# Optimization experiments

Hardware: AMD Instinct MI355X
Metric: run time of the kernel (lower is better)

Reference implementation:

```python
import jax, jax.numpy as jnp
import numpy as np

EPS = 1e-15
BN_EPS = 1e-5
N_NODES = 50000
N_EDGES = 800000
IN_CH = 32
OUT_CH = 32
DIM = 3


def _gmm_params(key, in_ch, out_ch, K):
    k1, k2, k3, k4 = jax.random.split(key, 4)
    g = jax.random.normal(k1, (in_ch, K * out_ch), jnp.float32) * (1.0 / np.sqrt(in_ch))
    mu = jax.random.normal(k2, (K, DIM), jnp.float32)
    sigma = jax.random.uniform(k3, (K, DIM), jnp.float32, 0.5, 1.5)
    root = jax.random.normal(k4, (in_ch, out_ch), jnp.float32) * (1.0 / np.sqrt(in_ch))
    bias = jnp.zeros((out_ch,), jnp.float32)
    return g, mu, sigma, root, bias


def setup_inputs() -> dict:
    key = jax.random.key(0)
    ks = jax.random.split(key, 12)
    x = jax.random.normal(ks[0], (N_NODES, IN_CH), jnp.float32)
    edge_index = jax.random.randint(ks[1], (2, N_EDGES), 0, N_NODES, jnp.int64)
    edge_attr = jax.random.uniform(ks[2], (N_EDGES, DIM), jnp.float32)
    g1, mu1, sig1, root1, b1 = _gmm_params(ks[3], IN_CH, OUT_CH, 5)
    g2, mu2, sig2, root2, b2 = _gmm_params(ks[4], OUT_CH, OUT_CH, 5)
    gs, mus, sigs, roots, bs = _gmm_params(ks[5], IN_CH, OUT_CH, 1)
    ones = jnp.ones((OUT_CH,), jnp.float32)
    zeros = jnp.zeros((OUT_CH,), jnp.float32)
    return dict(x=x, edge_attr=edge_attr,
                g1=g1, mu1=mu1, sig1=sig1, root1=root1, b1=b1, gam1=ones, bet1=zeros,
                g2=g2, mu2=mu2, sig2=sig2, root2=root2, b2=b2, gam2=ones, bet2=zeros,
                gs=gs, mus=mus, sigs=sigs, roots=roots, bs=bs, gams=ones, bets=zeros,
                edge_index=edge_index)


def gmm_conv(x, edge_index, edge_attr, g, mu, sigma, root, bias, num_nodes):
    # PyG GMMConv (separate kernels=False, aggr='mean', root_weight=True)
    src, dst = edge_index[0], edge_index[1]
    K = mu.shape[0]
    out_ch = root.shape[1]
    # Gaussian mixture weights per edge/kernel: [E, K]
    diff = edge_attr[:, None, :] - mu[None, :, :]               # [E, K, D]
    w = jnp.exp(jnp.sum(-0.5 * diff * diff / (EPS + sigma[None] ** 2), axis=-1))
    # Project and gather source features: [E, K, out]
    xj = (x @ g).reshape(-1, K, out_ch)[src] if False else (x[src] @ g).reshape(-1, K, out_ch)
    msg = jnp.einsum('ek,ekc->ec', w, xj)                        # [E, out]
    agg = jax.ops.segment_sum(msg, dst, num_segments=num_nodes)
    cnt = jax.ops.segment_sum(jnp.ones((msg.shape[0],), msg.dtype), dst, num_segments=num_nodes)
    agg = agg / jnp.maximum(cnt, 1.0)[:, None]                   # mean aggregation
    return agg + x @ root + bias


def batch_norm(x, gamma, beta):
    mean = jnp.mean(x, axis=0)
    var = jnp.var(x, axis=0)
    return gamma * (x - mean) * jax.lax.rsqrt(var + BN_EPS) + beta


def reference(x, edge_attr,
              g1, mu1, sig1, root1, b1, gam1, bet1,
              g2, mu2, sig2, root2, b2, gam2, bet2,
              gs, mus, sigs, roots, bs, gams, bets,
              edge_index):
    n = x.shape[0]
    h = jax.nn.elu(batch_norm(gmm_conv(x, edge_index, edge_attr, g1, mu1, sig1, root1, b1, n), gam1, bet1))
    h = batch_norm(gmm_conv(h, edge_index, edge_attr, g2, mu2, sig2, root2, b2, n), gam2, bet2)
    s = batch_norm(gmm_conv(x, edge_index, edge_attr, gs, mus, sigs, roots, bs, n), gams, bets)
    return jax.nn.elu(h + s)
```

## Files before the change

kernel.cpp:

```cpp
#include <hip/hip_runtime.h>
#include <hip/hip_fp16.h>
#include <math.h>

#define NN 50000
#define NE 800000
#define GEPS 1e-15f
#define BN_EPS 1e-5f
#define NB 196
#define LOG2E 1.4426950408889634f

typedef _Float16 f16x8 __attribute__((ext_vector_type(8)));
typedef float f32x4 __attribute__((ext_vector_type(4)));

__device__ __forceinline__ float2 h2f(unsigned int u) {
    __half2 h = *reinterpret_cast<const __half2*>(&u);
    return __half22float2(h);
}

__global__ void precompute_gc(const float* __restrict__ sig1, const float* __restrict__ mu1,
                              const float* __restrict__ sig2, const float* __restrict__ mu2,
                              const float* __restrict__ sigs, const float* __restrict__ mus,
                              float* __restrict__ gc) {
    int s = threadIdx.x;
    if (s >= 11) return;
    const float* sg; const float* mu;
    if (s < 5)       { sg = sig1 + s * 3;       mu = mu1 + s * 3; }
    else if (s < 10) { sg = sig2 + (s - 5) * 3; mu = mu2 + (s - 5) * 3; }
    else             { sg = sigs;               mu = mus; }
    float C = 0.f;
    for (int d = 0; d < 3; d++) {
        float sv = sg[d];
        float iv = -0.5f / (GEPS + sv * sv) * LOG2E;
        float m = mu[d];
        gc[s * 8 + d] = iv;
        gc[s * 8 + 3 + d] = -2.f * iv * m;
        C += iv * m * m;
    }
    gc[s * 8 + 6] = C;
    gc[s * 8 + 7] = 0.f;
}

__global__ void hist_kernel(const int* __restrict__ ei, int* __restrict__ deg) {
    int t = blockIdx.x * blockDim.x + threadIdx.x;
    int e0 = t * 4;
    if (e0 >= NE) return;
    int4 dv = *(const int4*)(ei + NE + e0);
    atomicAdd(&deg[dv.x], 1);
    atomicAdd(&deg[dv.y], 1);
    atomicAdd(&deg[dv.z], 1);
    atomicAdd(&deg[dv.w], 1);
}

__global__ void block_reduce_kernel(const int* __restrict__ deg, int* __restrict__ bsum) {
    __shared__ int sh[256];
    int t = threadIdx.x;
    int i = blockIdx.x * 256 + t;
    sh[t] = (i < NN) ? deg[i] : 0;
    __syncthreads();
    for (int off = 128; off > 0; off >>= 1) {
        if (t < off) sh[t] += sh[t + off];
        __syncthreads();
    }
    if (t == 0) bsum[blockIdx.x] = sh[0];
}

__global__ void scan_partials_kernel(int* __restrict__ bsum) {
    __shared__ int sh[256];
    int t = threadIdx.x;
    int v = (t < NB) ? bsum[t] : 0;
    sh[t] = v;
    __syncthreads();
    for (int off = 1; off < 256; off <<= 1) {
        int u = (t >= off) ? sh[t - off] : 0;
        __syncthreads();
        sh[t] += u;
        __syncthreads();
    }
    if (t < NB) bsum[t] = sh[t] - v;
}

__global__ void block_scan_kernel(const int* __restrict__ deg, const int* __restrict__ bsum,
                                  int* __restrict__ rowstart, int* __restrict__ cursor) {
    __shared__ int sh[256];
    int t = threadIdx.x;
    int i = blockIdx.x * 256 + t;
    int v = (i < NN) ? deg[i] : 0;
    sh[t] = v;
    __syncthreads();
    for (int off = 1; off < 256; off <<= 1) {
        int u = (t >= off) ? sh[t - off] : 0;
        __syncthreads();
        sh[t] += u;
        __syncthreads();
    }
    int excl = sh[t] - v + bsum[blockIdx.x];
    if (i < NN) { rowstart[i] = excl; cursor[i] = excl; }
}

__global__ void reorder_scatter(const int* __restrict__ ei, int* __restrict__ cursor,
                                int* __restrict__ perm) {
    int t = blockIdx.x * blockDim.x + threadIdx.x;
    int e0 = t * 4;
    if (e0 >= NE) return;
    int4 dv = *(const int4*)(ei + NE + e0);
    int p0 = atomicAdd(&cursor[dv.x], 1);
    int p1 = atomicAdd(&cursor[dv.y], 1);
    int p2 = atomicAdd(&cursor[dv.z], 1);
    int p3 = atomicAdd(&cursor[dv.w], 1);
    perm[p0] = e0;
    perm[p1] = e0 + 1;
    perm[p2] = e0 + 2;
    perm[p3] = e0 + 3;
}

__global__ void reorder_build(const int* __restrict__ perm, const int* __restrict__ ei,
                              const float* __restrict__ ea, const float* __restrict__ gc,
                              int4* __restrict__ recA, int4* __restrict__ recB) {
    int t = blockIdx.x * blockDim.x + threadIdx.x;
    int p0 = t * 4;
    if (p0 >= NE) return;
    int4 pv = *(const int4*)(perm + p0);
    int es[4] = {pv.x, pv.y, pv.z, pv.w};

    int   srcs[4];
    float av[4][3];
#pragma unroll
    for (int k = 0; k < 4; k++) {
        int e = es[k];
        srcs[k] = ei[e];
        av[k][0] = ea[e * 3 + 0];
        av[k][1] = ea[e * 3 + 1];
        av[k][2] = ea[e * 3 + 2];
    }

    int4 qa[4], qb[4];
#pragma unroll
    for (int k = 0; k < 4; k++) {
        float a0 = av[k][0], a1 = av[k][1], a2 = av[k][2];
        float s0 = a0 * a0, s1 = a1 * a1, s2 = a2 * a2;
        __half wv[11];
#pragma unroll
        for (int s = 0; s < 11; s++) {
            float ex = gc[s * 8 + 6];
            ex = fmaf(gc[s * 8 + 3], a0, ex);
            ex = fmaf(gc[s * 8 + 4], a1, ex);
            ex = fmaf(gc[s * 8 + 5], a2, ex);
            ex = fmaf(gc[s * 8 + 0], s0, ex);
            ex = fmaf(gc[s * 8 + 1], s1, ex);
            ex = fmaf(gc[s * 8 + 2], s2, ex);
            wv[s] = __float2half(exp2f(ex));
        }
        union UA { struct { int src; __half w[6]; } r; int4 q; } ua;
        ua.r.src = srcs[k];
        ua.r.w[0] = wv[0]; ua.r.w[1] = wv[1]; ua.r.w[2] = wv[2];
        ua.r.w[3] = wv[3]; ua.r.w[4] = wv[4]; ua.r.w[5] = wv[10];
        union UB { struct { int src; __half w[5]; __half pad; } r; int4 q; } ub;
        ub.r.src = srcs[k];
        ub.r.w[0] = wv[5]; ub.r.w[1] = wv[6]; ub.r.w[2] = wv[7];
        ub.r.w[3] = wv[8]; ub.r.w[4] = wv[9]; ub.r.pad = __float2half(0.f);
        qa[k] = ua.q;
        qb[k] = ub.q;
    }
#pragma unroll
    for (int k = 0; k < 4; k++) recA[p0 + k] = qa[k];
#pragma unroll
    for (int k = 0; k < 4; k++) recB[p0 + k] = qb[k];
}

__global__ void projR_kernel(const float* __restrict__ x, const float* __restrict__ root1,
                             const float* __restrict__ b1, const float* __restrict__ roots,
                             const float* __restrict__ bs, __half* __restrict__ xh,
                             float* __restrict__ R1, float* __restrict__ Rs) {
    const int t = threadIdx.x;
    const int col = t & 31;
    const int half_ = (t >> 5) & 1;
    const int rg = t >> 6;
    float w[32];
    const float* rootp = half_ ? roots : root1;
#pragma unroll
    for (int i = 0; i < 32; i++) w[i] = rootp[i * 32 + col];
    float b = half_ ? bs[col] : b1[col];
    float* Rp = half_ ? Rs : R1;
    __shared__ float hs[256];
    for (int n0 = blockIdx.x * 8; n0 < NN; n0 += gridDim.x * 8) {
        float v = x[(size_t)n0 * 32 + t];
        hs[t] = v;
        xh[(size_t)n0 * 32 + t] = __float2half(v);
        __syncthreads();
#pragma unroll
        for (int rr = 0; rr < 2; rr++) {
            int r = rg * 2 + rr;
            float acc = b;
#pragma unroll
            for (int i = 0; i < 32; i++) acc += w[i] * hs[r * 32 + i];
            Rp[(size_t)(n0 + r) * 32 + col] = acc;
        }
        __syncthreads();
    }
}

__global__ void projB2_kernel(const float* __restrict__ c1, const float* __restrict__ stats,
                              const float* __restrict__ gam1, const float* __restrict__ bet1,
                              const float* __restrict__ root2, const float* __restrict__ b2,
                              __half* __restrict__ hh, float* __restrict__ R2) {
    const int t = threadIdx.x;
    const int col = t & 31;
    const int rg = t >> 5;
    __shared__ float sc[32], sf[32];
    if (t < 32) {
        const float invN = 1.0f / (float)NN;
        float m = stats[t] * invN;
        float v = stats[32 + t] * invN - m * m;
        float s = gam1[t] * rsqrtf(v + BN_EPS);
        sc[t] = s;
        sf[t] = bet1[t] - m * s;
    }
    float w[32];
#pragma unroll
    for (int i = 0; i < 32; i++) w[i] = root2[i * 32 + col];
    float b = b2[col];
    __shared__ float hs[256];
    __syncthreads();
    for (int n0 = blockIdx.x * 8; n0 < NN; n0 += gridDim.x * 8) {
        float v = c1[(size_t)n0 * 32 + t];
        float hv = sc[t & 31] * v + sf[t & 31];
        hv = hv > 0.f ? hv : (__expf(hv) - 1.f);
        hs[t] = hv;
        hh[(size_t)n0 * 32 + t] = __float2half(hv);
        __syncthreads();
        float acc = b;
#pragma unroll
        for (int i = 0; i < 32; i++) acc += w[i] * hs[rg * 32 + i];
        R2[(size_t)(n0 + rg) * 32 + col] = acc;
        __syncthreads();
    }
}

template <bool SKIP>
__global__ void agg_kernel(const int4* __restrict__ rec, const int* __restrict__ rowstart,
                           const int* __restrict__ deg, const __half* __restrict__ X,
                           __half* __restrict__ Aout) {
    constexpr int NS = SKIP ? 6 : 5;
    constexpr int SA = SKIP ? 192 : 160;
    const int tid = blockIdx.x * blockDim.x + threadIdx.x;
    const int lane = threadIdx.x & 63;
    const int grp = lane >> 4;
    const int ch2 = lane & 15;
    const int wavesTotal = (gridDim.x * blockDim.x) >> 6;
    const int wid = tid >> 6;

    for (int n = wid; n < NN; n += wavesTotal) {
        const int start = rowstart[n];
        const int d = deg[n];
        float2 acc[NS];
#pragma unroll
        for (int s = 0; s < NS; s++) acc[s] = make_float2(0.f, 0.f);
        for (int i = grp; i < d; i += 4) {
            int4 r = rec[(size_t)(start + i)];
            const __half2 xv = *(const __half2*)(X + (((size_t)r.x) << 5) + 2 * ch2);
            float2 xf = __half22float2(xv);
            float2 w01 = h2f((unsigned)r.y);
            float2 w23 = h2f((unsigned)r.z);
            float2 w45 = h2f((unsigned)r.w);
            float wv[6] = {w01.x, w01.y, w23.x, w23.y, w45.x, w45.y};
#pragma unroll
            for (int s = 0; s < NS; s++) {
                acc[s].x = fmaf(wv[s], xf.x, acc[s].x);
                acc[s].y = fmaf(wv[s], xf.y, acc[s].y);
            }
        }
#pragma unroll
        for (int s = 0; s < NS; s++) {
            acc[s].x += __shfl_xor(acc[s].x, 16, 64);
            acc[s].x += __shfl_xor(acc[s].x, 32, 64);
            acc[s].y += __shfl_xor(acc[s].y, 16, 64);
            acc[s].y += __shfl_xor(acc[s].y, 32, 64);
        }
        if (grp == 0) {
            const float invd = 1.0f / fmaxf((float)d, 1.0f);
            __half* base = Aout + (size_t)n * SA + 2 * ch2;
#pragma unroll
            for (int s = 0; s < 5; s++) {
                __half2 hv = __floats2half2_rn(acc[s].x * invd, acc[s].y * invd);
                *(__half2*)(base + s * 32) = hv;
            }
            if (SKIP) {
                __half2 hv = __floats2half2_rn(acc[5].x * invd, acc[5].y * invd);
                *(__half2*)(base + 160) = hv;
            }
        }
    }
}

template <bool SKIP>
__global__ __launch_bounds__(256, 4) void gemm_kernel(
        const __half* __restrict__ Ah, const float* __restrict__ G,
        const float* __restrict__ Gs, const float* __restrict__ R,
        const float* __restrict__ Rs, float* __restrict__ C,
        float* __restrict__ Cs, float* __restrict__ stats) {
    constexpr int SA = SKIP ? 192 : 160;
    const int tid = blockIdx.x * blockDim.x + threadIdx.x;
    const int l = threadIdx.x & 63;
    const int r16 = l & 15;
    const int quad = l >> 4;
    const int wid = tid >> 6;
    const int nw = (gridDim.x * blockDim.x) >> 6;

    f16x8 bf[5][2];
#pragma unroll
    for (int kt = 0; kt < 5; kt++)
#pragma unroll
        for (int ct = 0; ct < 2; ct++)
#pragma unroll
            for (int e = 0; e < 8; e++) {
                int jj = quad * 8 + e;
                bf[kt][ct][e] = (_Float16)G[jj * 160 + kt * 32 + ct * 16 + r16];
            }
    f16x8 bs[2];
    if (SKIP) {
#pragma unroll
        for (int ct = 0; ct < 2; ct++)
#pragma unroll
            for (int e = 0; e < 8; e++) {
                int jj = quad * 8 + e;
                bs[ct][e] = (_Float16)Gs[jj * 32 + ct * 16 + r16];
            }
    }

    float s0 = 0.f, s1 = 0.f, q0 = 0.f, q1 = 0.f;
    float t0 = 0.f, t1 = 0.f, u0 = 0.f, u1 = 0.f;

    for (int tile = wid; tile < NN / 16; tile += nw) {
        const int n0 = tile * 16;
        const __half* arow = Ah + (size_t)(n0 + r16) * SA + quad * 8;
        f32x4 acc0 = {0.f, 0.f, 0.f, 0.f};
        f32x4 acc1 = {0.f, 0.f, 0.f, 0.f};
        f32x4 sa0 = {0.f, 0.f, 0.f, 0.f};
        f32x4 sa1 = {0.f, 0.f, 0.f, 0.f};
#pragma unroll
        for (int kt = 0; kt < 5; kt++) {
            f16x8 a = *(const f16x8*)(arow + kt * 32);
            acc0 = __builtin_amdgcn_mfma_f32_16x16x32_f16(a, bf[kt][0], acc0, 0, 0, 0);
            acc1 = __builtin_amdgcn_mfma_f32_16x16x32_f16(a, bf[kt][1], acc1, 0, 0, 0);
        }
        if (SKIP) {
            f16x8 a = *(const f16x8*)(arow + 160);
            sa0 = __builtin_amdgcn_mfma_f32_16x16x32_f16(a, bs[0], sa0, 0, 0, 0);
            sa1 = __builtin_amdgcn_mfma_f32_16x16x32_f16(a, bs[1], sa1, 0, 0, 0);
        }
#pragma unroll
        for (int r = 0; r < 4; r++) {
            const int nr = n0 + quad * 4 + r;
            const int b = nr * 32;
            {
                float v = acc0[r] + R[b + r16];
                C[b + r16] = v; s0 += v; q0 += v * v;
            }
            {
                float v = acc1[r] + R[b + 16 + r16];
                C[b + 16 + r16] = v; s1 += v; q1 += v * v;
            }
            if (SKIP) {
                float v = sa0[r] + Rs[b + r16];
                Cs[b + r16] = v; t0 += v; u0 += v * v;
                float w2 = sa1[r] + Rs[b + 16 + r16];
                Cs[b + 16 + r16] = w2; t1 += w2; u1 += w2 * w2;
            }
        }
    }
    s0 += __shfl_xor(s0, 16, 64); s0 += __shfl_xor(s0, 32, 64);
    s1 += __shfl_xor(s1, 16, 64); s1 += __shfl_xor(s1, 32, 64);
    q0 += __shfl_xor(q0, 16, 64); q0 += __shfl_xor(q0, 32, 64);
    q1 += __shfl_xor(q1, 16, 64); q1 += __shfl_xor(q1, 32, 64);
    if (SKIP) {
        t0 += __shfl_xor(t0, 16, 64); t0 += __shfl_xor(t0, 32, 64);
        t1 += __shfl_xor(t1, 16, 64); t1 += __shfl_xor(t1, 32, 64);
        u0 += __shfl_xor(u0, 16, 64); u0 += __shfl_xor(u0, 32, 64);
        u1 += __shfl_xor(u1, 16, 64); u1 += __shfl_xor(u1, 32, 64);
    }
    __shared__ float sred[128];
    const int t = threadIdx.x;
    if (t < 128) sred[t] = 0.f;
    __syncthreads();
    if (l < 16) {
        atomicAdd(&sred[l], s0);       atomicAdd(&sred[16 + l], s1);
        atomicAdd(&sred[32 + l], q0);  atomicAdd(&sred[48 + l], q1);
        if (SKIP) {
            atomicAdd(&sred[64 + l], t0);  atomicAdd(&sred[80 + l], t1);
            atomicAdd(&sred[96 + l], u0);  atomicAdd(&sred[112 + l], u1);
        }
    }
    __syncthreads();
    if (SKIP) { if (t < 128) atomicAdd(&stats[t], sred[t]); }
    else      { if (t < 64)  atomicAdd(&stats[t], sred[t]); }
}

__global__ void apply2_kernel(const float* __restrict__ c2, const float* __restrict__ cs,
                              const float* __restrict__ stats, const float* __restrict__ gam2,
                              const float* __restrict__ bet2, const float* __restrict__ gams,
                              const float* __restrict__ bets, float* __restrict__ out) {
    int idx = blockIdx.x * blockDim.x + threadIdx.x;
    if (idx >= NN * 32) return;
    int ch = idx & 31;
    const float invN = 1.0f / (float)NN;
    float m2 = stats[128 + ch] * invN;
    float v2 = stats[160 + ch] * invN - m2 * m2;
    float ms = stats[64 + ch] * invN;
    float vs = stats[96 + ch] * invN - ms * ms;
    float bn2 = gam2[ch] * (c2[idx] - m2) * rsqrtf(v2 + BN_EPS) + bet2[ch];
    float bns = gams[ch] * (cs[idx] - ms) * rsqrtf(vs + BN_EPS) + bets[ch];
    float o = bn2 + bns;
    out[idx] = o > 0.f ? o : (__expf(o) - 1.f);
}

extern "C" void kernel_launch(void* const* d_in, const int* in_sizes, int n_in,
                              void* d_out, int out_size, void* d_ws, size_t ws_size,
                              hipStream_t stream) {
    const float* x     = (const float*)d_in[0];
    const float* ea    = (const float*)d_in[1];
    const float* g1    = (const float*)d_in[2];
    const float* mu1   = (const float*)d_in[3];
    const float* sig1  = (const float*)d_in[4];
    const float* root1 = (const float*)d_in[5];
    const float* b1    = (const float*)d_in[6];
    const float* gam1  = (const float*)d_in[7];
    const float* bet1  = (const float*)d_in[8];
    const float* g2    = (const float*)d_in[9];
    const float* mu2   = (const float*)d_in[10];
    const float* sig2  = (const float*)d_in[11];
    const float* root2 = (const float*)d_in[12];
    const float* b2    = (const float*)d_in[13];
    const float* gam2  = (const float*)d_in[14];
    const float* bet2  = (const float*)d_in[15];
    const float* gs    = (const float*)d_in[16];
    const float* mus   = (const float*)d_in[17];
    const float* sigs  = (const float*)d_in[18];
    const float* roots = (const float*)d_in[19];
    const float* bs    = (const float*)d_in[20];
    const float* gams  = (const float*)d_in[21];
    const float* bets  = (const float*)d_in[22];
    const int*   ei    = (const int*)d_in[23];
    float* out = (float*)d_out;

    char* w = (char*)d_ws;
    __half* xh  = (__half*)w;   w += (size_t)NN * 32 * 2;
    __half* hh  = (__half*)w;   w += (size_t)NN * 32 * 2;
    __half* Ah  = (__half*)w;   w += (size_t)NN * 192 * 2;
    float*  R1  = (float*)w;    w += (size_t)NN * 32 * 4;
    float*  Rs  = (float*)w;    w += (size_t)NN * 32 * 4;
    float*  R2  = (float*)w;    w += (size_t)NN * 32 * 4;
    float*  c1  = (float*)w;    w += (size_t)NN * 32 * 4;
    float*  cs  = (float*)w;    w += (size_t)NN * 32 * 4;
    int4*   recA = (int4*)w;    w += (size_t)NE * 16;
    int4*   recB = (int4*)w;    w += (size_t)NE * 16;
    int*    perm = (int*)w;     w += (size_t)NE * 4;
    int*    deg = (int*)w;      w += (size_t)NN * 4;
    int*    rowstart = (int*)w; w += (size_t)NN * 4;
    int*    cursor   = (int*)w; w += (size_t)NN * 4;
    int*    bsum = (int*)w;     w += 256 * 4;
    float*  stats = (float*)w;  w += 256 * 4;
    float*  gc    = (float*)w;  w += 11 * 8 * 4;

    const int ilpBlocks   = (NE / 4 + 255) / 256;
    const int applyBlocks = (NN * 32 + 255) / 256;

    hipMemsetAsync(deg, 0, NN * sizeof(int), stream);
    hipMemsetAsync(stats, 0, 256 * sizeof(float), stream);
    precompute_gc<<<1, 16, 0, stream>>>(sig1, mu1, sig2, mu2, sigs, mus, gc);

    hist_kernel<<<ilpBlocks, 256, 0, stream>>>(ei, deg);
    block_reduce_kernel<<<NB, 256, 0, stream>>>(deg, bsum);
    scan_partials_kernel<<<1, 256, 0, stream>>>(bsum);
    block_scan_kernel<<<NB, 256, 0, stream>>>(deg, bsum, rowstart, cursor);
    reorder_scatter<<<ilpBlocks, 256, 0, stream>>>(ei, cursor, perm);
    reorder_build<<<ilpBlocks, 256, 0, stream>>>(perm, ei, ea, gc, recA, recB);

    projR_kernel<<<1024, 256, 0, stream>>>(x, root1, b1, roots, bs, xh, R1, Rs);
    agg_kernel<true><<<2048, 256, 0, stream>>>(recA, rowstart, deg, xh, Ah);
    gemm_kernel<true><<<512, 256, 0, stream>>>(Ah, g1, gs, R1, Rs, c1, cs, stats);

    projB2_kernel<<<1024, 256, 0, stream>>>(c1, stats, gam1, bet1, root2, b2, hh, R2);
    agg_kernel<false><<<2048, 256, 0, stream>>>(recB, rowstart, deg, hh, Ah);
    gemm_kernel<false><<<512, 256, 0, stream>>>(Ah, g2, nullptr, R2, nullptr, c1, nullptr,
                                                stats + 128);
    apply2_kernel<<<applyBlocks, 256, 0, stream>>>(c1, cs, stats, gam2, bet2, gams, bets, out);
}
```

Before: 351.7 us.

## Record per-edge rank in histogram pass and scatter CSR perm per XCD

The histogram pass now keeps the atomicAdd return value as each edge's rank within its destination, so the second atomic pass over a cursor array goes away. The scatter kernel becomes a plain write to rowstart[dst]+rank. That scatter is split into 8 groups by blockIdx&7, each group writing only destinations in its own node range, so writes to a given perm region tend to come from a single XCD's L2. The cost is an extra rank array written and read, and every group re-reads the full edge list.

```diff
diff --git a/kernel.cpp b/kernel.cpp
--- a/kernel.cpp
+++ b/kernel.cpp
@@ -8,6 +8,7 @@
 #define BN_EPS 1e-5f
 #define NB 196
 #define LOG2E 1.4426950408889634f
+#define NODES_PER_XCD 6250
 
 typedef _Float16 f16x8 __attribute__((ext_vector_type(8)));
 typedef float f32x4 __attribute__((ext_vector_type(4)));
@@ -40,15 +41,18 @@
     gc[s * 8 + 7] = 0.f;
 }
 
-__global__ void hist_kernel(const int* __restrict__ ei, int* __restrict__ deg) {
+__global__ void rank_kernel(const int* __restrict__ ei, int* __restrict__ deg,
+                            int* __restrict__ rankv) {
     int t = blockIdx.x * blockDim.x + threadIdx.x;
     int e0 = t * 4;
     if (e0 >= NE) return;
     int4 dv = *(const int4*)(ei + NE + e0);
-    atomicAdd(&deg[dv.x], 1);
-    atomicAdd(&deg[dv.y], 1);
-    atomicAdd(&deg[dv.z], 1);
-    atomicAdd(&deg[dv.w], 1);
+    int4 rv;
+    rv.x = atomicAdd(&deg[dv.x], 1);
+    rv.y = atomicAdd(&deg[dv.y], 1);
+    rv.z = atomicAdd(&deg[dv.z], 1);
+    rv.w = atomicAdd(&deg[dv.w], 1);
+    *(int4*)(rankv + e0) = rv;
 }
 
 __global__ void block_reduce_kernel(const int* __restrict__ deg, int* __restrict__ bsum) {
@@ -80,7 +84,7 @@
 }
 
 __global__ void block_scan_kernel(const int* __restrict__ deg, const int* __restrict__ bsum,
-                                  int* __restrict__ rowstart, int* __restrict__ cursor) {
+                                  int* __restrict__ rowstart) {
     __shared__ int sh[256];
     int t = threadIdx.x;
     int i = blockIdx.x * 256 + t;
@@ -94,23 +98,23 @@
         __syncthreads();
     }
     int excl = sh[t] - v + bsum[blockIdx.x];
-    if (i < NN) { rowstart[i] = excl; cursor[i] = excl; }
-}
-
-__global__ void reorder_scatter(const int* __restrict__ ei, int* __restrict__ cursor,
-                                int* __restrict__ perm) {
-    int t = blockIdx.x * blockDim.x + threadIdx.x;
-    int e0 = t * 4;
-    if (e0 >= NE) return;
-    int4 dv = *(const int4*)(ei + NE + e0);
-    int p0 = atomicAdd(&cursor[dv.x], 1);
-    int p1 = atomicAdd(&cursor[dv.y], 1);
-    int p2 = atomicAdd(&cursor[dv.z], 1);
-    int p3 = atomicAdd(&cursor[dv.w], 1);
-    perm[p0] = e0;
-    perm[p1] = e0 + 1;
-    perm[p2] = e0 + 2;
-    perm[p3] = e0 + 3;
+    if (i < NN) rowstart[i] = excl;
+}
+
+__global__ void scatter_xcd(const int* __restrict__ ei, const int* __restrict__ rankv,
+                            const int* __restrict__ rowstart, int* __restrict__ perm) {
+    const int g = blockIdx.x & 7;
+    const int v = blockIdx.x >> 3;
+    const int VB = gridDim.x >> 3;
+    const int stride = VB * blockDim.x * 4;
+    for (int e0 = (v * blockDim.x + threadIdx.x) * 4; e0 < NE; e0 += stride) {
+        int4 dv = *(const int4*)(ei + NE + e0);
+        int4 rv = *(const int4*)(rankv + e0);
+        if (dv.x / NODES_PER_XCD == g) perm[rowstart[dv.x] + rv.x] = e0;
+        if (dv.y / NODES_PER_XCD == g) perm[rowstart[dv.y] + rv.y] = e0 + 1;
+        if (dv.z / NODES_PER_XCD == g) perm[rowstart[dv.z] + rv.z] = e0 + 2;
+        if (dv.w / NODES_PER_XCD == g) perm[rowstart[dv.w] + rv.w] = e0 + 3;
+    }
 }
 
 __global__ void reorder_build(const int* __restrict__ perm, const int* __restrict__ ei,
@@ -454,9 +458,9 @@
     int4*   recA = (int4*)w;    w += (size_t)NE * 16;
     int4*   recB = (int4*)w;    w += (size_t)NE * 16;
     int*    perm = (int*)w;     w += (size_t)NE * 4;
+    int*    rankv = (int*)w;    w += (size_t)NE * 4;
     int*    deg = (int*)w;      w += (size_t)NN * 4;
     int*    rowstart = (int*)w; w += (size_t)NN * 4;
-    int*    cursor   = (int*)w; w += (size_t)NN * 4;
     int*    bsum = (int*)w;     w += 256 * 4;
     float*  stats = (float*)w;  w += 256 * 4;
     float*  gc    = (float*)w;  w += 11 * 8 * 4;
@@ -468,11 +472,11 @@
     hipMemsetAsync(stats, 0, 256 * sizeof(float), stream);
     precompute_gc<<<1, 16, 0, stream>>>(sig1, mu1, sig2, mu2, sigs, mus, gc);
 
-    hist_kernel<<<ilpBlocks, 256, 0, stream>>>(ei, deg);
+    rank_kernel<<<ilpBlocks, 256, 0, stream>>>(ei, deg, rankv);
     block_reduce_kernel<<<NB, 256, 0, stream>>>(deg, bsum);
     scan_partials_kernel<<<1, 256, 0, stream>>>(bsum);
-    block_scan_kernel<<<NB, 256, 0, stream>>>(deg, bsum, rowstart, cursor);
-    reorder_scatter<<<ilpBlocks, 256, 0, stream>>>(ei, cursor, perm);
+    block_scan_kernel<<<NB, 256, 0, stream>>>(deg, bsum, rowstart);
+    scatter_xcd<<<1024, 256, 0, stream>>>(ei, rankv, rowstart, perm);
     reorder_build<<<ilpBlocks, 256, 0, stream>>>(perm, ei, ea, gc, recA, recB);
 
     projR_kernel<<<1024, 256, 0, stream>>>(x, root1, b1, roots, bs, xh, R1, Rs);
```

Result: faster. 315.0 us (-10.4%).
